# Performance work log

Hardware: AMD Instinct MI355X
Metric: run time of the kernel (lower is better)

Reference implementation:

```python
import jax, jax.numpy as jnp
import numpy as np

DELTA_VAR = 0.5
DELTA_DIST = 1.5
LOSS_WEIGHT = 1.0
L_MAX = 17  # segment ids 0..16 (0 = background)
EPS = 1e-12


def setup_inputs() -> dict:
    key = jax.random.key(0)
    k1, k2 = jax.random.split(key)
    B, D, H, W = 16, 16, 288, 512
    emb = jax.random.normal(k1, (B, D, H, W), dtype=jnp.float32)
    seg = jax.random.randint(k2, (B, 1, H, W), 0, L_MAX, dtype=jnp.int64)
    return {"input": emb, "target": seg}


def _per_image_losses(e, s):
    # e: [D, N] float, s: [N] int labels in [0, L_MAX)
    D, N = e.shape
    et = e.T  # [N, D]
    cnt = jax.ops.segment_sum(jnp.ones((N,), e.dtype), s, num_segments=L_MAX)  # [L]
    sums = jax.ops.segment_sum(et, s, num_segments=L_MAX)                      # [L, D]
    present = (cnt > 0) & (jnp.arange(L_MAX) != 0)
    num_lanes = jnp.sum(present).astype(e.dtype)
    means = sums / jnp.maximum(cnt, 1.0)[:, None]                              # [L, D]

    # variance (pull) term: per-pixel distance to own-label centroid
    diff = et - means[s]                                                       # [N, D]
    nrm = jnp.sqrt(jnp.maximum(jnp.sum(diff * diff, axis=1), EPS))             # [N]
    term = jax.nn.relu(nrm - DELTA_VAR) ** 2
    per_label = jax.ops.segment_sum(term, s, num_segments=L_MAX) / jnp.maximum(cnt, 1.0)
    var_l = jnp.sum(jnp.where(present, per_label, 0.0)) / jnp.maximum(num_lanes, 1.0)
    var_l = jnp.where(num_lanes > 0, var_l, 0.0)

    # distance (push) term: pairwise centroid distances among present lanes
    d = means[:, None, :] - means[None, :, :]                                  # [L, L, D]
    sumsq = jnp.sum(d * d, axis=2)                                             # [L, L]
    pair_mask = present[:, None] & present[None, :] & ~jnp.eye(L_MAX, dtype=bool)
    dist = jnp.sqrt(jnp.where(pair_mask, sumsq, 1.0))
    push = jnp.sum(jnp.where(pair_mask, jax.nn.relu(DELTA_DIST - dist) ** 2, 0.0))
    denom = jnp.maximum(num_lanes * (num_lanes - 1.0), 1.0)
    dist_l = jnp.where(num_lanes > 1, push / denom / 2.0, 0.0)
    return var_l, dist_l


def reference(input, target):
    B, D, H, W = input.shape
    N = H * W
    emb = input.reshape(B, D, N)
    seg = target.reshape(B, N).astype(jnp.int32)
    var_l, dist_l = jax.vmap(_per_image_losses)(emb, seg)
    loss = (jnp.sum(var_l) + jnp.sum(dist_l)) / B
    return loss * LOSS_WEIGHT
```

## Files before the change

kernel.cpp:

```cpp
#include <hip/hip_runtime.h>

#define BB  16
#define DD  16
#define NN  (288*512)
#define LL  17
#define QPI (NN/4)
#define PB  48
#define PXB (NN/PB)
#define TILE 1024
#define TPB 256


__global__ __launch_bounds__(TPB) void k_accum(const float* __restrict__ emb,
                                               const int* __restrict__ seg,
                                               float* __restrict__ part) {
    __shared__ int slab[TILE];
    const int tid  = threadIdx.x;
    const int b    = blockIdx.y;
    const int blk  = blockIdx.x;
    const int dgrp = tid >> 6;
    const int j    = tid & 63;
    const float* embb = emb + (size_t)b * DD * NN;
    const int*   segb = seg + (size_t)b * NN;
    const int base0 = blk * PXB;

    float a0[LL], a1[LL], a2[LL], a3[LL], cf[LL];
#pragma unroll
    for (int l = 0; l < LL; ++l) { a0[l]=0.f; a1[l]=0.f; a2[l]=0.f; a3[l]=0.f; cf[l]=0.f; }

    const float* r0 = embb + (size_t)(dgrp*4+0) * NN;
    const float* r1 = embb + (size_t)(dgrp*4+1) * NN;
    const float* r2 = embb + (size_t)(dgrp*4+2) * NN;
    const float* r3 = embb + (size_t)(dgrp*4+3) * NN;

    for (int t = 0; t < PXB / TILE; ++t) {
        const int tb = base0 + t * TILE;
        *(int4*)(slab + tid * 4) = *(const int4*)(segb + tb + tid * 4);
        __syncthreads();
#pragma unroll
        for (int s = 0; s < TILE / 256; ++s) {
            const int p = s * 256 + j * 4;
            const int4   s4 = *(const int4*)(slab + p);
            const float4 e0 = *(const float4*)(r0 + tb + p);
            const float4 e1 = *(const float4*)(r1 + tb + p);
            const float4 e2 = *(const float4*)(r2 + tb + p);
            const float4 e3 = *(const float4*)(r3 + tb + p);
#pragma unroll
            for (int l = 0; l < LL; ++l) {
                const float mx = (s4.x == l) ? 1.f : 0.f;
                const float my = (s4.y == l) ? 1.f : 0.f;
                const float mz = (s4.z == l) ? 1.f : 0.f;
                const float mw = (s4.w == l) ? 1.f : 0.f;
                a0[l] = fmaf(mx, e0.x, fmaf(my, e0.y, fmaf(mz, e0.z, fmaf(mw, e0.w, a0[l]))));
                a1[l] = fmaf(mx, e1.x, fmaf(my, e1.y, fmaf(mz, e1.z, fmaf(mw, e1.w, a1[l]))));
                a2[l] = fmaf(mx, e2.x, fmaf(my, e2.y, fmaf(mz, e2.z, fmaf(mw, e2.w, a2[l]))));
                a3[l] = fmaf(mx, e3.x, fmaf(my, e3.y, fmaf(mz, e3.z, fmaf(mw, e3.w, a3[l]))));
            }
            if (dgrp == 0) {
#pragma unroll
                for (int l = 0; l < LL; ++l)
                    cf[l] += ((s4.x==l)?1.f:0.f) + ((s4.y==l)?1.f:0.f)
                           + ((s4.z==l)?1.f:0.f) + ((s4.w==l)?1.f:0.f);
            }
        }
        __syncthreads();
    }

    float* pp = part + ((size_t)b * PB + blk) * 289;
#pragma unroll
    for (int l = 0; l < LL; ++l) {
        float v0 = a0[l], v1 = a1[l], v2 = a2[l], v3 = a3[l];
#pragma unroll
        for (int off = 32; off; off >>= 1) {
            v0 += __shfl_down(v0, off, 64);
            v1 += __shfl_down(v1, off, 64);
            v2 += __shfl_down(v2, off, 64);
            v3 += __shfl_down(v3, off, 64);
        }
        if (j == 0) {
            pp[l*16 + dgrp*4 + 0] = v0;
            pp[l*16 + dgrp*4 + 1] = v1;
            pp[l*16 + dgrp*4 + 2] = v2;
            pp[l*16 + dgrp*4 + 3] = v3;
        }
        float c = cf[l];
#pragma unroll
        for (int off = 32; off; off >>= 1) c += __shfl_down(c, off, 64);
        if (tid == 0) pp[272 + l] = c;
    }
}

__global__ __launch_bounds__(64) void k_stats(const float* __restrict__ part,
                                              float* __restrict__ gmean,
                                              float* __restrict__ gw,
                                              float* __restrict__ dvec) {
    __shared__ float mm[289];
    const int tid = threadIdx.x;
    const int b = blockIdx.x;
    for (int i = tid; i < 289; i += 64) {
        const int l = i / 17, d = i % 17;
        const int isrc = (d < 16) ? (l * 16 + d) : (272 + l);
        float v = 0.f;
        for (int p = 0; p < PB; ++p) v += part[((size_t)b * PB + p) * 289 + isrc];
        mm[i] = v;
    }
    __syncthreads();
    for (int i = tid; i < 272; i += 64) {
        const int l = i >> 4, d = i & 15;
        const float c = mm[l * 17 + 16];
        const float mv = mm[l * 17 + d] / fmaxf(c, 1.f);
        mm[l * 17 + d] = mv;
        gmean[(size_t)b * 272 + i] = mv;
    }
    __syncthreads();

    int nl = 0;
#pragma unroll
    for (int l = 1; l < LL; ++l) nl += (mm[l * 17 + 16] > 0.f) ? 1 : 0;
    const float nlf = (float)nl;

    if (tid < LL) {
        const bool pres = (tid != 0) && (mm[tid * 17 + 16] > 0.f);
        gw[(size_t)b * 17 + tid] = pres
            ? 1.f / (fmaxf(mm[tid * 17 + 16], 1.f) * fmaxf(nlf, 1.f) * (float)BB) : 0.f;
    }

    float push = 0.f;
    for (int p = tid; p < 289; p += 64) {
        const int i = p / 17, jj = p % 17;
        if (i != jj && i > 0 && jj > 0 && mm[i*17+16] > 0.f && mm[jj*17+16] > 0.f) {
            float ss = 0.f;
#pragma unroll
            for (int d = 0; d < DD; ++d) {
                const float df = mm[i*17+d] - mm[jj*17+d];
                ss += df * df;
            }
            const float t = fmaxf(1.5f - sqrtf(ss), 0.f);
            push += t * t;
        }
    }
#pragma unroll
    for (int off = 32; off; off >>= 1) push += __shfl_down(push, off, 64);
    if (tid == 0)
        dvec[b] = (nl > 1) ? push / (fmaxf(nlf * (nlf - 1.f), 1.f) * 2.f * (float)BB) : 0.f;
}

__global__ __launch_bounds__(TPB) void k_var(const float* __restrict__ emb,
                                             const int* __restrict__ seg,
                                             const float* __restrict__ gmean,
                                             const float* __restrict__ gw,
                                             float* __restrict__ vpart) {
    __shared__ float m[289];
    __shared__ float wl[17];
    __shared__ float wsum[TPB / 64];
    const int tid = threadIdx.x;
    const int b = blockIdx.y;
    for (int i = tid; i < 272; i += TPB)
        m[(i >> 4) * 17 + (i & 15)] = gmean[(size_t)b * 272 + i];
    if (tid < LL) wl[tid] = gw[(size_t)b * 17 + tid];
    __syncthreads();

    const float* embb = emb + (size_t)b * DD * NN;
    const int*   segb = seg + (size_t)b * NN;
    float accl = 0.f;

    for (int q = blockIdx.x * TPB + tid; q < QPI; q += PB * TPB) {
        const int n = q * 4;
        const int4 s4 = *(const int4*)(segb + n);
        const int o0 = s4.x * 17, o1 = s4.y * 17, o2 = s4.z * 17, o3 = s4.w * 17;
        float ss0 = 0.f, ss1 = 0.f, ss2 = 0.f, ss3 = 0.f;
#pragma unroll
        for (int d = 0; d < DD; ++d) {
            const float4 e = *(const float4*)(embb + (size_t)d * NN + n);
            const float d0 = e.x - m[o0 + d]; ss0 += d0 * d0;
            const float d1 = e.y - m[o1 + d]; ss1 += d1 * d1;
            const float d2 = e.z - m[o2 + d]; ss2 += d2 * d2;
            const float d3 = e.w - m[o3 + d]; ss3 += d3 * d3;
        }
        float t;
        t = fmaxf(sqrtf(fmaxf(ss0, 1e-12f)) - 0.5f, 0.f); accl += t * t * wl[s4.x];
        t = fmaxf(sqrtf(fmaxf(ss1, 1e-12f)) - 0.5f, 0.f); accl += t * t * wl[s4.y];
        t = fmaxf(sqrtf(fmaxf(ss2, 1e-12f)) - 0.5f, 0.f); accl += t * t * wl[s4.z];
        t = fmaxf(sqrtf(fmaxf(ss3, 1e-12f)) - 0.5f, 0.f); accl += t * t * wl[s4.w];
    }
#pragma unroll
    for (int off = 32; off; off >>= 1) accl += __shfl_down(accl, off, 64);
    if ((tid & 63) == 0) wsum[tid >> 6] = accl;
    __syncthreads();
    if (tid == 0)
        vpart[(size_t)b * PB + blockIdx.x] = wsum[0] + wsum[1] + wsum[2] + wsum[3];
}

__global__ __launch_bounds__(TPB) void k_final(const float* __restrict__ vpart,
                                               const float* __restrict__ dvec,
                                               float* __restrict__ out) {
    __shared__ float ws4[TPB / 64];
    float v = 0.f;
    for (int i = threadIdx.x; i < BB * PB; i += TPB) v += vpart[i];
    if (threadIdx.x < BB) v += dvec[threadIdx.x];
#pragma unroll
    for (int off = 32; off; off >>= 1) v += __shfl_down(v, off, 64);
    if ((threadIdx.x & 63) == 0) ws4[threadIdx.x >> 6] = v;
    __syncthreads();
    if (threadIdx.x == 0) out[0] = ws4[0] + ws4[1] + ws4[2] + ws4[3];
}

extern "C" void kernel_launch(void* const* d_in, const int* in_sizes, int n_in,
                              void* d_out, int out_size, void* d_ws, size_t ws_size,
                              hipStream_t stream) {
    const float* emb = (const float*)d_in[0];
    const int*   seg = (const int*)d_in[1];
    float* out = (float*)d_out;

    float* part  = (float*)d_ws;
    float* gmean = part + BB * PB * 289;
    float* gw    = gmean + BB * 272;
    float* dvec  = gw + BB * 17;
    float* vpart = dvec + BB;

    k_accum<<<dim3(PB, BB), TPB, 0, stream>>>(emb, seg, part);
    k_stats<<<BB, 64, 0, stream>>>(part, gmean, gw, dvec);
    k_var  <<<dim3(PB, BB), TPB, 0, stream>>>(emb, seg, gmean, gw, vpart);
    k_final<<<1, TPB, 0, stream>>>(vpart, dvec, out);
}
```

Measured before the change: 282.2 us.

## Replace masked per-label FMA accumulation with fixed-point LDS atomic histograms

The segment-sum kernel now scatters each pixel's embedding into replicated shared-memory tables with integer atomics on values scaled to 32768ths, instead of running a 17-label masked FMA loop per pixel. Block results go to a global int accumulator through atomics after a memset, so the stats kernel reads one summed value and no longer reduces per-block partials. The variance kernel uses one 4-pixel group per thread over more blocks instead of a grid-stride loop. This removes most of the ALU work in accumulation, at the cost of fixed-point rounding error, possible int overflow at larger scales, and contention on the LDS atomics.

```diff
diff --git a/kernel.cpp b/kernel.cpp
--- a/kernel.cpp
+++ b/kernel.cpp
@@ -1,41 +1,47 @@
 #include <hip/hip_runtime.h>
 
-#define BB  16
-#define DD  16
-#define NN  (288*512)
-#define LL  17
-#define QPI (NN/4)
-#define PB  48
-#define PXB (NN/PB)
-#define TILE 1024
-#define TPB 256
+#define BB   16
+#define DD   16
+#define NN   (288*512)
+#define LL   17
+#define TPB  256
+#define PB   96
+#define PXB  (NN/PB)
+#define TILE 512
+#define PBV  144
+#define NREP 16
+
+#define FSCALE 32768.0f
+#define INV_FSCALE (1.0f/32768.0f)
 
 
 __global__ __launch_bounds__(TPB) void k_accum(const float* __restrict__ emb,
                                                const int* __restrict__ seg,
-                                               float* __restrict__ part) {
+                                               int* __restrict__ acc) {
     __shared__ int slab[TILE];
+    __shared__ int tab[NREP * 289];
     const int tid  = threadIdx.x;
     const int b    = blockIdx.y;
     const int blk  = blockIdx.x;
     const int dgrp = tid >> 6;
     const int j    = tid & 63;
+    int* trep = tab + (j & (NREP - 1)) * 289;
+
+    for (int i = tid; i < NREP * 289; i += TPB) tab[i] = 0;
+
     const float* embb = emb + (size_t)b * DD * NN;
     const int*   segb = seg + (size_t)b * NN;
     const int base0 = blk * PXB;
-
-    float a0[LL], a1[LL], a2[LL], a3[LL], cf[LL];
-#pragma unroll
-    for (int l = 0; l < LL; ++l) { a0[l]=0.f; a1[l]=0.f; a2[l]=0.f; a3[l]=0.f; cf[l]=0.f; }
-
-    const float* r0 = embb + (size_t)(dgrp*4+0) * NN;
-    const float* r1 = embb + (size_t)(dgrp*4+1) * NN;
-    const float* r2 = embb + (size_t)(dgrp*4+2) * NN;
-    const float* r3 = embb + (size_t)(dgrp*4+3) * NN;
+    const float* r0 = embb + (size_t)(dgrp * 4 + 0) * NN;
+    const float* r1 = embb + (size_t)(dgrp * 4 + 1) * NN;
+    const float* r2 = embb + (size_t)(dgrp * 4 + 2) * NN;
+    const float* r3 = embb + (size_t)(dgrp * 4 + 3) * NN;
+    __syncthreads();
 
     for (int t = 0; t < PXB / TILE; ++t) {
         const int tb = base0 + t * TILE;
-        *(int4*)(slab + tid * 4) = *(const int4*)(segb + tb + tid * 4);
+        if (tid < TILE / 4)
+            *(int4*)(slab + tid * 4) = *(const int4*)(segb + tb + tid * 4);
         __syncthreads();
 #pragma unroll
         for (int s = 0; s < TILE / 256; ++s) {
@@ -45,52 +51,45 @@
             const float4 e1 = *(const float4*)(r1 + tb + p);
             const float4 e2 = *(const float4*)(r2 + tb + p);
             const float4 e3 = *(const float4*)(r3 + tb + p);
-#pragma unroll
-            for (int l = 0; l < LL; ++l) {
-                const float mx = (s4.x == l) ? 1.f : 0.f;
-                const float my = (s4.y == l) ? 1.f : 0.f;
-                const float mz = (s4.z == l) ? 1.f : 0.f;
-                const float mw = (s4.w == l) ? 1.f : 0.f;
-                a0[l] = fmaf(mx, e0.x, fmaf(my, e0.y, fmaf(mz, e0.z, fmaf(mw, e0.w, a0[l]))));
-                a1[l] = fmaf(mx, e1.x, fmaf(my, e1.y, fmaf(mz, e1.z, fmaf(mw, e1.w, a1[l]))));
-                a2[l] = fmaf(mx, e2.x, fmaf(my, e2.y, fmaf(mz, e2.z, fmaf(mw, e2.w, a2[l]))));
-                a3[l] = fmaf(mx, e3.x, fmaf(my, e3.y, fmaf(mz, e3.z, fmaf(mw, e3.w, a3[l]))));
-            }
+            const int o0 = s4.x * 17 + dgrp * 4;
+            const int o1 = s4.y * 17 + dgrp * 4;
+            const int o2 = s4.z * 17 + dgrp * 4;
+            const int o3 = s4.w * 17 + dgrp * 4;
+            atomicAdd(trep + o0 + 0, __float2int_rn(e0.x * FSCALE));
+            atomicAdd(trep + o0 + 1, __float2int_rn(e1.x * FSCALE));
+            atomicAdd(trep + o0 + 2, __float2int_rn(e2.x * FSCALE));
+            atomicAdd(trep + o0 + 3, __float2int_rn(e3.x * FSCALE));
+            atomicAdd(trep + o1 + 0, __float2int_rn(e0.y * FSCALE));
+            atomicAdd(trep + o1 + 1, __float2int_rn(e1.y * FSCALE));
+            atomicAdd(trep + o1 + 2, __float2int_rn(e2.y * FSCALE));
+            atomicAdd(trep + o1 + 3, __float2int_rn(e3.y * FSCALE));
+            atomicAdd(trep + o2 + 0, __float2int_rn(e0.z * FSCALE));
+            atomicAdd(trep + o2 + 1, __float2int_rn(e1.z * FSCALE));
+            atomicAdd(trep + o2 + 2, __float2int_rn(e2.z * FSCALE));
+            atomicAdd(trep + o2 + 3, __float2int_rn(e3.z * FSCALE));
+            atomicAdd(trep + o3 + 0, __float2int_rn(e0.w * FSCALE));
+            atomicAdd(trep + o3 + 1, __float2int_rn(e1.w * FSCALE));
+            atomicAdd(trep + o3 + 2, __float2int_rn(e2.w * FSCALE));
+            atomicAdd(trep + o3 + 3, __float2int_rn(e3.w * FSCALE));
             if (dgrp == 0) {
-#pragma unroll
-                for (int l = 0; l < LL; ++l)
-                    cf[l] += ((s4.x==l)?1.f:0.f) + ((s4.y==l)?1.f:0.f)
-                           + ((s4.z==l)?1.f:0.f) + ((s4.w==l)?1.f:0.f);
+                atomicAdd(trep + s4.x * 17 + 16, 1);
+                atomicAdd(trep + s4.y * 17 + 16, 1);
+                atomicAdd(trep + s4.z * 17 + 16, 1);
+                atomicAdd(trep + s4.w * 17 + 16, 1);
             }
         }
         __syncthreads();
     }
 
-    float* pp = part + ((size_t)b * PB + blk) * 289;
-#pragma unroll
-    for (int l = 0; l < LL; ++l) {
-        float v0 = a0[l], v1 = a1[l], v2 = a2[l], v3 = a3[l];
-#pragma unroll
-        for (int off = 32; off; off >>= 1) {
-            v0 += __shfl_down(v0, off, 64);
-            v1 += __shfl_down(v1, off, 64);
-            v2 += __shfl_down(v2, off, 64);
-            v3 += __shfl_down(v3, off, 64);
-        }
-        if (j == 0) {
-            pp[l*16 + dgrp*4 + 0] = v0;
-            pp[l*16 + dgrp*4 + 1] = v1;
-            pp[l*16 + dgrp*4 + 2] = v2;
-            pp[l*16 + dgrp*4 + 3] = v3;
-        }
-        float c = cf[l];
-#pragma unroll
-        for (int off = 32; off; off >>= 1) c += __shfl_down(c, off, 64);
-        if (tid == 0) pp[272 + l] = c;
-    }
-}
-
-__global__ __launch_bounds__(64) void k_stats(const float* __restrict__ part,
+    for (int i = tid; i < 289; i += TPB) {
+        int v = 0;
+#pragma unroll
+        for (int r = 0; r < NREP; ++r) v += tab[r * 289 + i];
+        atomicAdd(acc + b * 289 + i, v);
+    }
+}
+
+__global__ __launch_bounds__(64) void k_stats(const int* __restrict__ acc,
                                               float* __restrict__ gmean,
                                               float* __restrict__ gw,
                                               float* __restrict__ dvec) {
@@ -98,11 +97,8 @@
     const int tid = threadIdx.x;
     const int b = blockIdx.x;
     for (int i = tid; i < 289; i += 64) {
-        const int l = i / 17, d = i % 17;
-        const int isrc = (d < 16) ? (l * 16 + d) : (272 + l);
-        float v = 0.f;
-        for (int p = 0; p < PB; ++p) v += part[((size_t)b * PB + p) * 289 + isrc];
-        mm[i] = v;
+        const int raw = acc[b * 289 + i];
+        mm[i] = (i % 17 == 16) ? (float)raw : (float)raw * INV_FSCALE;
     }
     __syncthreads();
     for (int i = tid; i < 272; i += 64) {
@@ -162,33 +158,31 @@
 
     const float* embb = emb + (size_t)b * DD * NN;
     const int*   segb = seg + (size_t)b * NN;
-    float accl = 0.f;
-
-    for (int q = blockIdx.x * TPB + tid; q < QPI; q += PB * TPB) {
-        const int n = q * 4;
-        const int4 s4 = *(const int4*)(segb + n);
-        const int o0 = s4.x * 17, o1 = s4.y * 17, o2 = s4.z * 17, o3 = s4.w * 17;
-        float ss0 = 0.f, ss1 = 0.f, ss2 = 0.f, ss3 = 0.f;
-#pragma unroll
-        for (int d = 0; d < DD; ++d) {
-            const float4 e = *(const float4*)(embb + (size_t)d * NN + n);
-            const float d0 = e.x - m[o0 + d]; ss0 += d0 * d0;
-            const float d1 = e.y - m[o1 + d]; ss1 += d1 * d1;
-            const float d2 = e.z - m[o2 + d]; ss2 += d2 * d2;
-            const float d3 = e.w - m[o3 + d]; ss3 += d3 * d3;
-        }
-        float t;
-        t = fmaxf(sqrtf(fmaxf(ss0, 1e-12f)) - 0.5f, 0.f); accl += t * t * wl[s4.x];
-        t = fmaxf(sqrtf(fmaxf(ss1, 1e-12f)) - 0.5f, 0.f); accl += t * t * wl[s4.y];
-        t = fmaxf(sqrtf(fmaxf(ss2, 1e-12f)) - 0.5f, 0.f); accl += t * t * wl[s4.z];
-        t = fmaxf(sqrtf(fmaxf(ss3, 1e-12f)) - 0.5f, 0.f); accl += t * t * wl[s4.w];
-    }
+
+    const int n = blockIdx.x * (TPB * 4) + tid * 4;
+    const int4 s4 = *(const int4*)(segb + n);
+    const int o0 = s4.x * 17, o1 = s4.y * 17, o2 = s4.z * 17, o3 = s4.w * 17;
+    float ss0 = 0.f, ss1 = 0.f, ss2 = 0.f, ss3 = 0.f;
+#pragma unroll
+    for (int d = 0; d < DD; ++d) {
+        const float4 e = *(const float4*)(embb + (size_t)d * NN + n);
+        const float d0 = e.x - m[o0 + d]; ss0 += d0 * d0;
+        const float d1 = e.y - m[o1 + d]; ss1 += d1 * d1;
+        const float d2 = e.z - m[o2 + d]; ss2 += d2 * d2;
+        const float d3 = e.w - m[o3 + d]; ss3 += d3 * d3;
+    }
+    float accl = 0.f, t;
+    t = fmaxf(sqrtf(fmaxf(ss0, 1e-12f)) - 0.5f, 0.f); accl += t * t * wl[s4.x];
+    t = fmaxf(sqrtf(fmaxf(ss1, 1e-12f)) - 0.5f, 0.f); accl += t * t * wl[s4.y];
+    t = fmaxf(sqrtf(fmaxf(ss2, 1e-12f)) - 0.5f, 0.f); accl += t * t * wl[s4.z];
+    t = fmaxf(sqrtf(fmaxf(ss3, 1e-12f)) - 0.5f, 0.f); accl += t * t * wl[s4.w];
+
 #pragma unroll
     for (int off = 32; off; off >>= 1) accl += __shfl_down(accl, off, 64);
     if ((tid & 63) == 0) wsum[tid >> 6] = accl;
     __syncthreads();
     if (tid == 0)
-        vpart[(size_t)b * PB + blockIdx.x] = wsum[0] + wsum[1] + wsum[2] + wsum[3];
+        vpart[(size_t)b * PBV + blockIdx.x] = wsum[0] + wsum[1] + wsum[2] + wsum[3];
 }
 
 __global__ __launch_bounds__(TPB) void k_final(const float* __restrict__ vpart,
@@ -196,7 +190,7 @@
                                                float* __restrict__ out) {
     __shared__ float ws4[TPB / 64];
     float v = 0.f;
-    for (int i = threadIdx.x; i < BB * PB; i += TPB) v += vpart[i];
+    for (int i = threadIdx.x; i < BB * PBV; i += TPB) v += vpart[i];
     if (threadIdx.x < BB) v += dvec[threadIdx.x];
 #pragma unroll
     for (int off = 32; off; off >>= 1) v += __shfl_down(v, off, 64);
@@ -212,14 +206,16 @@
     const int*   seg = (const int*)d_in[1];
     float* out = (float*)d_out;
 
-    float* part  = (float*)d_ws;
-    float* gmean = part + BB * PB * 289;
+    int*   acc   = (int*)d_ws;
+    float* gmean = (float*)(acc + BB * 289);
     float* gw    = gmean + BB * 272;
     float* dvec  = gw + BB * 17;
     float* vpart = dvec + BB;
 
-    k_accum<<<dim3(PB, BB), TPB, 0, stream>>>(emb, seg, part);
-    k_stats<<<BB, 64, 0, stream>>>(part, gmean, gw, dvec);
-    k_var  <<<dim3(PB, BB), TPB, 0, stream>>>(emb, seg, gmean, gw, vpart);
+    hipMemsetAsync(acc, 0, (size_t)BB * 289 * sizeof(int), stream);
+
+    k_accum<<<dim3(PB, BB), TPB, 0, stream>>>(emb, seg, acc);
+    k_stats<<<BB, 64, 0, stream>>>(acc, gmean, gw, dvec);
+    k_var  <<<dim3(PBV, BB), TPB, 0, stream>>>(emb, seg, gmean, gw, vpart);
     k_final<<<1, TPB, 0, stream>>>(vpart, dvec, out);
 }
```

After: 252.4 us. 1.12x faster.
